# Performance work log

Hardware: AMD Instinct MI355X
Metric: run time of the kernel (lower is better)

## Reference

```python
import jax, jax.numpy as jnp
import numpy as np

THR = 0.2
BORDER_RM = 2
TEMPERATURE = 0.1


def _border_valid(hc, wc, b):
    # True for grid cells at least b away from every border; flattened to [hc*wc]
    ih = jnp.arange(hc)
    iw = jnp.arange(wc)
    vh = (ih >= b) & (ih < hc - b)
    vw = (iw >= b) & (iw < wc - b)
    return (vh[:, None] & vw[None, :]).reshape(-1)


def setup_inputs() -> dict:
    key = jax.random.key(0)
    k0, k1 = jax.random.split(key)
    N, C = 4, 256
    h0c = w0c = h1c = w1c = 64  # 512/8 coarse grid
    feat_c0 = jax.random.normal(k0, (N, h0c * w0c, C), dtype=jnp.float32)
    feat_c1 = jax.random.normal(k1, (N, h1c * w1c, C), dtype=jnp.float32)
    return {"feat_c0": feat_c0, "feat_c1": feat_c1,
            "h0c": h0c, "w0c": w0c, "h1c": h1c, "w1c": w1c}


def reference(feat_c0, feat_c1, h0c, w0c, h1c, w1c):
    C = feat_c0.shape[-1]
    inv_sqrt_c = 1.0 / np.sqrt(C)
    f0 = feat_c0 * inv_sqrt_c
    f1 = feat_c1 * inv_sqrt_c
    # [N, L, S] similarity, dual softmax
    sim = jnp.einsum('nlc,nsc->nls', f0, f1) / TEMPERATURE
    conf = jax.nn.softmax(sim, axis=1) * jax.nn.softmax(sim, axis=2)
    # threshold + border suppression (eval path: mask_border)
    mask = conf > THR
    v0 = _border_valid(h0c, w0c, BORDER_RM)  # [L]
    v1 = _border_valid(h1c, w1c, BORDER_RM)  # [S]
    mask = mask & v0[None, :, None] & v1[None, None, :]
    # mutual top-1 (argmax along both rows and columns)
    mask = mask & (conf == conf.max(axis=2, keepdims=True)) \
                & (conf == conf.max(axis=1, keepdims=True))
    # per-row match: padded fixed-shape form of torch.where(mask_v)
    mask_v = mask.any(axis=2)                     # [N, L] bool: row i has a match
    j_ids = jnp.argmax(mask, axis=2)              # [N, L] matched column (0 if none)
    mconf = jnp.take_along_axis(conf, j_ids[..., None], axis=2)[..., 0]
    mconf = jnp.where(mask_v, mconf, 0.0)         # zero where no match (== m_bids filter)
    return conf, mask_v, j_ids.astype(jnp.int32), mconf
```

## Files before the change

kernel.cpp:

```cpp
#include <hip/hip_runtime.h>

#define L_DIM 4096
#define C_DIM 256
#define NB 4

typedef __bf16 bf16x8 __attribute__((ext_vector_type(8)));
typedef float f32x4 __attribute__((ext_vector_type(4)));

#define GLB __attribute__((address_space(1)))
#define AS3 __attribute__((address_space(3)))

__global__ void init_ws(float* __restrict__ rsum, float* __restrict__ csum,
                        unsigned int* __restrict__ colmax,
                        unsigned long long* __restrict__ rowpack) {
    int i = blockIdx.x * 256 + threadIdx.x;
    if (i < NB * L_DIM) { rsum[i] = 0.f; csum[i] = 0.f; colmax[i] = 0u; rowpack[i] = 0ull; }
}

__global__ __launch_bounds__(256) void conv_k(const float* __restrict__ f0,
                                              const float* __restrict__ f1,
                                              __bf16* __restrict__ abf,
                                              __bf16* __restrict__ bbf) {
    int i = blockIdx.x * 256 + threadIdx.x;
    const float* in = blockIdx.y ? f1 : f0;
    __bf16* out = blockIdx.y ? bbf : abf;
    const float4* p = (const float4*)in + (size_t)i * 2;
    float4 a = p[0], b = p[1];
    bf16x8 v;
    v[0]=(__bf16)a.x; v[1]=(__bf16)a.y; v[2]=(__bf16)a.z; v[3]=(__bf16)a.w;
    v[4]=(__bf16)b.x; v[5]=(__bf16)b.y; v[6]=(__bf16)b.z; v[7]=(__bf16)b.w;
    *(bf16x8*)&out[(size_t)i * 8] = v;
}

template<bool PRE, int MODE>
__global__ __launch_bounds__(256) void gemm_pass(
        const float* __restrict__ f0, const float* __restrict__ f1,
        const __bf16* __restrict__ a_bf, const __bf16* __restrict__ b_bf,
        float* __restrict__ E,
        float* __restrict__ rsum, float* __restrict__ csum,
        unsigned long long* __restrict__ rowpack, unsigned int* __restrict__ colmax) {
    const int n  = blockIdx.z;
    const int tl = blockIdx.y;
    const int ts = blockIdx.x;

    constexpr int LDST = PRE ? 64 : 72;
    __shared__ __bf16 Al[128 * LDST];
    __shared__ __bf16 Bl[128 * LDST];

    const int t    = threadIdx.x;
    const int lane = t & 63;
    const int wave = t >> 6;
    const int wm   = wave >> 1, wn = wave & 1;
    const int q    = lane >> 4;
    const int l15  = lane & 15;

    const float* A = f0 + ((size_t)n * L_DIM + (size_t)tl * 128) * C_DIM;
    const float* B = f1 + ((size_t)n * L_DIM + (size_t)ts * 128) * C_DIM;
    const __bf16* gA = a_bf + ((size_t)n * L_DIM + (size_t)tl * 128) * C_DIM;
    const __bf16* gB = b_bf + ((size_t)n * L_DIM + (size_t)ts * 128) * C_DIM;

    f32x4 acc[4][4] = {};

    const int r8 = t >> 3;
    const int c8 = t & 7;
    const int lr = lane >> 3;
    const int lc = ((lane & 7) ^ lr) * 8;

    for (int kt = 0; kt < C_DIM; kt += 64) {
        if constexpr (PRE) {
            #pragma unroll
            for (int i = 0; i < 4; ++i) {
                const int chunk = wave * 4 + i;
                const int row = chunk * 8 + lr;
                __builtin_amdgcn_global_load_lds(
                    (const GLB void*)(gA + (size_t)row * C_DIM + kt + lc),
                    (AS3 void*)&Al[chunk * 512], 16, 0, 0);
                __builtin_amdgcn_global_load_lds(
                    (const GLB void*)(gB + (size_t)row * C_DIM + kt + lc),
                    (AS3 void*)&Bl[chunk * 512], 16, 0, 0);
            }
        } else {
            #pragma unroll
            for (int i = 0; i < 4; ++i) {
                int row = r8 + 32 * i;
                const float4* pa = (const float4*)(A + (size_t)row * C_DIM + kt + c8 * 8);
                float4 a0 = pa[0], a1 = pa[1];
                const float4* pb = (const float4*)(B + (size_t)row * C_DIM + kt + c8 * 8);
                float4 b0 = pb[0], b1 = pb[1];
                bf16x8 av, bv;
                av[0]=(__bf16)a0.x; av[1]=(__bf16)a0.y; av[2]=(__bf16)a0.z; av[3]=(__bf16)a0.w;
                av[4]=(__bf16)a1.x; av[5]=(__bf16)a1.y; av[6]=(__bf16)a1.z; av[7]=(__bf16)a1.w;
                bv[0]=(__bf16)b0.x; bv[1]=(__bf16)b0.y; bv[2]=(__bf16)b0.z; bv[3]=(__bf16)b0.w;
                bv[4]=(__bf16)b1.x; bv[5]=(__bf16)b1.y; bv[6]=(__bf16)b1.z; bv[7]=(__bf16)b1.w;
                *(bf16x8*)&Al[row * LDST + c8 * 8] = av;
                *(bf16x8*)&Bl[row * LDST + c8 * 8] = bv;
            }
        }
        __syncthreads();
        #pragma unroll
        for (int k2 = 0; k2 < 2; ++k2) {
            int off;
            if constexpr (PRE) off = ((k2 * 4 + q) ^ (l15 & 7)) * 8;
            else               off = k2 * 32 + q * 8;
            bf16x8 af[4], bfv[4];
            #pragma unroll
            for (int mf = 0; mf < 4; ++mf)
                af[mf] = *(const bf16x8*)&Al[(wm * 64 + mf * 16 + l15) * LDST + off];
            #pragma unroll
            for (int nf = 0; nf < 4; ++nf)
                bfv[nf] = *(const bf16x8*)&Bl[(wn * 64 + nf * 16 + l15) * LDST + off];
            #pragma unroll
            for (int mf = 0; mf < 4; ++mf)
                #pragma unroll
                for (int nf = 0; nf < 4; ++nf)
                    acc[mf][nf] = __builtin_amdgcn_mfma_f32_16x16x32_bf16(
                        af[mf], bfv[nf], acc[mf][nf], 0, 0, 0);
        }
        __syncthreads();
    }

    if constexpr (MODE == 0) {
        const float scale = 0.0390625f;
        #pragma unroll
        for (int mf = 0; mf < 4; ++mf)
            #pragma unroll
            for (int nf = 0; nf < 4; ++nf)
                #pragma unroll
                for (int reg = 0; reg < 4; ++reg)
                    acc[mf][nf][reg] = __expf(acc[mf][nf][reg] * scale);

        {
            float rp[4][4];
            #pragma unroll
            for (int mf = 0; mf < 4; ++mf)
                #pragma unroll
                for (int reg = 0; reg < 4; ++reg) {
                    float v = acc[mf][0][reg] + acc[mf][1][reg] + acc[mf][2][reg] + acc[mf][3][reg];
                    v += __shfl_xor(v, 1); v += __shfl_xor(v, 2);
                    v += __shfl_xor(v, 4); v += __shfl_xor(v, 8);
                    rp[mf][reg] = v;
                }
            if (l15 == 0) {
                #pragma unroll
                for (int mf = 0; mf < 4; ++mf)
                    #pragma unroll
                    for (int reg = 0; reg < 4; ++reg)
                        atomicAdd(&rsum[n * L_DIM + tl * 128 + wm * 64 + mf * 16 + q * 4 + reg],
                                  rp[mf][reg]);
            }
        }
        {
            float cp[4];
            #pragma unroll
            for (int nf = 0; nf < 4; ++nf) {
                float v = 0.f;
                #pragma unroll
                for (int mf = 0; mf < 4; ++mf)
                    #pragma unroll
                    for (int reg = 0; reg < 4; ++reg)
                        v += acc[mf][nf][reg];
                v += __shfl_xor(v, 16); v += __shfl_xor(v, 32);
                cp[nf] = v;
            }
            if (q == 0) {
                #pragma unroll
                for (int nf = 0; nf < 4; ++nf)
                    atomicAdd(&csum[n * L_DIM + ts * 128 + wn * 64 + nf * 16 + l15], cp[nf]);
            }
        }
    } else {
        const float scale2 = 0.078125f;
        float vr[4][4];
        #pragma unroll
        for (int mf = 0; mf < 4; ++mf)
            #pragma unroll
            for (int reg = 0; reg < 4; ++reg)
                vr[mf][reg] = 1.0f / rsum[n * L_DIM + tl * 128 + wm * 64 + mf * 16 + q * 4 + reg];
        float vc[4];
        #pragma unroll
        for (int nf = 0; nf < 4; ++nf)
            vc[nf] = 1.0f / csum[n * L_DIM + ts * 128 + wn * 64 + nf * 16 + l15];

        #pragma unroll
        for (int mf = 0; mf < 4; ++mf)
            #pragma unroll
            for (int nf = 0; nf < 4; ++nf)
                #pragma unroll
                for (int reg = 0; reg < 4; ++reg)
                    acc[mf][nf][reg] =
                        __expf(acc[mf][nf][reg] * scale2) * vr[mf][reg] * vc[nf];

        float* Eb = E + (size_t)n * L_DIM * L_DIM + (size_t)tl * 128 * L_DIM + (size_t)ts * 128;
        #pragma unroll
        for (int mf = 0; mf < 4; ++mf) {
            #pragma unroll
            for (int nf = 0; nf < 4; ++nf) {
                int col = wn * 64 + nf * 16 + l15;
                #pragma unroll
                for (int reg = 0; reg < 4; ++reg) {
                    int row = wm * 64 + mf * 16 + q * 4 + reg;
                    Eb[(size_t)row * L_DIM + col] = acc[mf][nf][reg];
                }
            }
        }

        #pragma unroll
        for (int mf = 0; mf < 4; ++mf) {
            #pragma unroll
            for (int reg = 0; reg < 4; ++reg) {
                unsigned long long best = 0ull;
                #pragma unroll
                for (int nf = 0; nf < 4; ++nf) {
                    unsigned int cb = __float_as_uint(acc[mf][nf][reg]);
                    unsigned int col = (unsigned int)(ts * 128 + wn * 64 + nf * 16 + l15);
                    unsigned long long p = ((unsigned long long)cb << 32) | (unsigned int)(~col);
                    best = p > best ? p : best;
                }
                #pragma unroll
                for (int m = 1; m < 16; m <<= 1) {
                    unsigned int hi = (unsigned int)(best >> 32), lo = (unsigned int)best;
                    hi = __shfl_xor(hi, m); lo = __shfl_xor(lo, m);
                    unsigned long long o = ((unsigned long long)hi << 32) | lo;
                    best = o > best ? o : best;
                }
                if (l15 == 0)
                    atomicMax(&rowpack[n * L_DIM + tl * 128 + wm * 64 + mf * 16 + q * 4 + reg],
                              best);
            }
        }
        #pragma unroll
        for (int nf = 0; nf < 4; ++nf) {
            float m0 = acc[0][nf][0];
            #pragma unroll
            for (int mf = 0; mf < 4; ++mf)
                #pragma unroll
                for (int reg = 0; reg < 4; ++reg)
                    m0 = fmaxf(m0, acc[mf][nf][reg]);
            unsigned int cb = __float_as_uint(m0);
            unsigned int o = __shfl_xor(cb, 16); cb = o > cb ? o : cb;
            o = __shfl_xor(cb, 32); cb = o > cb ? o : cb;
            if (q == 0)
                atomicMax(&colmax[n * L_DIM + ts * 128 + wn * 64 + nf * 16 + l15], cb);
        }
    }
}

__global__ void final_k(const unsigned long long* __restrict__ rowpack,
                        const unsigned int* __restrict__ colmax,
                        float* __restrict__ mask_out, float* __restrict__ j_out,
                        float* __restrict__ mconf_out) {
    int i = blockIdx.x * 256 + threadIdx.x;
    if (i >= NB * L_DIM) return;
    int n = i >> 12, l = i & 4095;
    unsigned long long rp = rowpack[i];
    float v = __uint_as_float((unsigned int)(rp >> 32));
    int s = (int)(~(unsigned int)(rp & 0xFFFFFFFFull));
    float cv = __uint_as_float(colmax[n * L_DIM + s]);
    int lh = l >> 6, lw = l & 63;
    int sh = s >> 6, sw = s & 63;
    bool bl = (lh >= 2) && (lh < 62) && (lw >= 2) && (lw < 62);
    bool bs = (sh >= 2) && (sh < 62) && (sw >= 2) && (sw < 62);
    bool m = (v > 0.2f) && bl && bs && (v == cv);
    mask_out[i]  = m ? 1.0f : 0.0f;
    j_out[i]     = m ? (float)s : 0.0f;
    mconf_out[i] = m ? v : 0.0f;
}

extern "C" void kernel_launch(void* const* d_in, const int* in_sizes, int n_in,
                              void* d_out, int out_size, void* d_ws, size_t ws_size,
                              hipStream_t stream) {
    const float* f0 = (const float*)d_in[0];
    const float* f1 = (const float*)d_in[1];

    float* out_conf  = (float*)d_out;
    float* out_mask  = out_conf + (size_t)NB * L_DIM * L_DIM;
    float* out_j     = out_mask + NB * L_DIM;
    float* out_mconf = out_j + NB * L_DIM;

    float* rsum = (float*)d_ws;
    float* csum = rsum + NB * L_DIM;
    unsigned int* colmax = (unsigned int*)(csum + NB * L_DIM);
    unsigned long long* rowpack = (unsigned long long*)(colmax + NB * L_DIM);
    __bf16* abf = (__bf16*)(rowpack + NB * L_DIM);
    __bf16* bbf = abf + (size_t)NB * L_DIM * C_DIM;

    size_t need = (size_t)(NB * L_DIM) * 20
                + 2 * (size_t)NB * L_DIM * C_DIM * sizeof(__bf16);
    bool pre = ws_size >= need;

    init_ws<<<dim3(64), dim3(256), 0, stream>>>(rsum, csum, colmax, rowpack);
    if (pre) {
        conv_k<<<dim3(2048, 2), dim3(256), 0, stream>>>(f0, f1, abf, bbf);
        gemm_pass<true, 0><<<dim3(32, 32, NB), dim3(256), 0, stream>>>(
            f0, f1, abf, bbf, nullptr, rsum, csum, nullptr, nullptr);
        gemm_pass<true, 1><<<dim3(32, 32, NB), dim3(256), 0, stream>>>(
            f0, f1, abf, bbf, out_conf, rsum, csum, rowpack, colmax);
    } else {
        gemm_pass<false, 0><<<dim3(32, 32, NB), dim3(256), 0, stream>>>(
            f0, f1, nullptr, nullptr, nullptr, rsum, csum, nullptr, nullptr);
        gemm_pass<false, 1><<<dim3(32, 32, NB), dim3(256), 0, stream>>>(
            f0, f1, nullptr, nullptr, out_conf, rsum, csum, rowpack, colmax);
    }
    final_k<<<dim3(64), dim3(256), 0, stream>>>(rowpack, colmax, out_mask, out_j, out_mconf);
}
```

Before: 455.8 us.

## Transpose MFMA operands for vectorized conf stores and fuse workspace zeroing

Swaps the A/B operands of the bf16 MFMA so each lane owns four consecutive columns, enabling 16-byte vector stores of the large conf output and reshuffling the row/column reductions and atomics to match. Workspace zeroing moves into the conversion kernel, dropping a launch, and the fp32 fallback path is removed. Reciprocals use the fast rcp builtin, trading slight precision for fewer instructions.

```diff
diff --git a/kernel.cpp b/kernel.cpp
--- a/kernel.cpp
+++ b/kernel.cpp
@@ -10,18 +10,16 @@
 #define GLB __attribute__((address_space(1)))
 #define AS3 __attribute__((address_space(3)))
 
-__global__ void init_ws(float* __restrict__ rsum, float* __restrict__ csum,
-                        unsigned int* __restrict__ colmax,
-                        unsigned long long* __restrict__ rowpack) {
-    int i = blockIdx.x * 256 + threadIdx.x;
-    if (i < NB * L_DIM) { rsum[i] = 0.f; csum[i] = 0.f; colmax[i] = 0u; rowpack[i] = 0ull; }
-}
-
 __global__ __launch_bounds__(256) void conv_k(const float* __restrict__ f0,
                                               const float* __restrict__ f1,
                                               __bf16* __restrict__ abf,
-                                              __bf16* __restrict__ bbf) {
+                                              __bf16* __restrict__ bbf,
+                                              float* __restrict__ ws_zero) {
     int i = blockIdx.x * 256 + threadIdx.x;
+    if (blockIdx.y == 0 && blockIdx.x < 80) {
+        int j = (blockIdx.x * 256 + threadIdx.x) * 4;
+        *(f32x4*)&ws_zero[j] = (f32x4){0.f, 0.f, 0.f, 0.f};
+    }
     const float* in = blockIdx.y ? f1 : f0;
     __bf16* out = blockIdx.y ? bbf : abf;
     const float4* p = (const float4*)in + (size_t)i * 2;
@@ -32,20 +30,18 @@
     *(bf16x8*)&out[(size_t)i * 8] = v;
 }
 
-template<bool PRE, int MODE>
+template<int MODE>
 __global__ __launch_bounds__(256) void gemm_pass(
-        const float* __restrict__ f0, const float* __restrict__ f1,
         const __bf16* __restrict__ a_bf, const __bf16* __restrict__ b_bf,
         float* __restrict__ E,
         float* __restrict__ rsum, float* __restrict__ csum,
         unsigned long long* __restrict__ rowpack, unsigned int* __restrict__ colmax) {
+    const int ts = blockIdx.x;
+    const int tl = blockIdx.y;
     const int n  = blockIdx.z;
-    const int tl = blockIdx.y;
-    const int ts = blockIdx.x;
-
-    constexpr int LDST = PRE ? 64 : 72;
-    __shared__ __bf16 Al[128 * LDST];
-    __shared__ __bf16 Bl[128 * LDST];
+
+    __shared__ __bf16 Al[128 * 64];
+    __shared__ __bf16 Bl[128 * 64];
 
     const int t    = threadIdx.x;
     const int lane = t & 63;
@@ -54,67 +50,43 @@
     const int q    = lane >> 4;
     const int l15  = lane & 15;
 
-    const float* A = f0 + ((size_t)n * L_DIM + (size_t)tl * 128) * C_DIM;
-    const float* B = f1 + ((size_t)n * L_DIM + (size_t)ts * 128) * C_DIM;
     const __bf16* gA = a_bf + ((size_t)n * L_DIM + (size_t)tl * 128) * C_DIM;
     const __bf16* gB = b_bf + ((size_t)n * L_DIM + (size_t)ts * 128) * C_DIM;
 
     f32x4 acc[4][4] = {};
 
-    const int r8 = t >> 3;
-    const int c8 = t & 7;
     const int lr = lane >> 3;
     const int lc = ((lane & 7) ^ lr) * 8;
 
     for (int kt = 0; kt < C_DIM; kt += 64) {
-        if constexpr (PRE) {
-            #pragma unroll
-            for (int i = 0; i < 4; ++i) {
-                const int chunk = wave * 4 + i;
-                const int row = chunk * 8 + lr;
-                __builtin_amdgcn_global_load_lds(
-                    (const GLB void*)(gA + (size_t)row * C_DIM + kt + lc),
-                    (AS3 void*)&Al[chunk * 512], 16, 0, 0);
-                __builtin_amdgcn_global_load_lds(
-                    (const GLB void*)(gB + (size_t)row * C_DIM + kt + lc),
-                    (AS3 void*)&Bl[chunk * 512], 16, 0, 0);
-            }
-        } else {
-            #pragma unroll
-            for (int i = 0; i < 4; ++i) {
-                int row = r8 + 32 * i;
-                const float4* pa = (const float4*)(A + (size_t)row * C_DIM + kt + c8 * 8);
-                float4 a0 = pa[0], a1 = pa[1];
-                const float4* pb = (const float4*)(B + (size_t)row * C_DIM + kt + c8 * 8);
-                float4 b0 = pb[0], b1 = pb[1];
-                bf16x8 av, bv;
-                av[0]=(__bf16)a0.x; av[1]=(__bf16)a0.y; av[2]=(__bf16)a0.z; av[3]=(__bf16)a0.w;
-                av[4]=(__bf16)a1.x; av[5]=(__bf16)a1.y; av[6]=(__bf16)a1.z; av[7]=(__bf16)a1.w;
-                bv[0]=(__bf16)b0.x; bv[1]=(__bf16)b0.y; bv[2]=(__bf16)b0.z; bv[3]=(__bf16)b0.w;
-                bv[4]=(__bf16)b1.x; bv[5]=(__bf16)b1.y; bv[6]=(__bf16)b1.z; bv[7]=(__bf16)b1.w;
-                *(bf16x8*)&Al[row * LDST + c8 * 8] = av;
-                *(bf16x8*)&Bl[row * LDST + c8 * 8] = bv;
-            }
+        #pragma unroll
+        for (int i = 0; i < 4; ++i) {
+            const int chunk = wave * 4 + i;
+            const int row = chunk * 8 + lr;
+            __builtin_amdgcn_global_load_lds(
+                (const GLB void*)(gA + (size_t)row * C_DIM + kt + lc),
+                (AS3 void*)&Al[chunk * 512], 16, 0, 0);
+            __builtin_amdgcn_global_load_lds(
+                (const GLB void*)(gB + (size_t)row * C_DIM + kt + lc),
+                (AS3 void*)&Bl[chunk * 512], 16, 0, 0);
         }
         __syncthreads();
         #pragma unroll
         for (int k2 = 0; k2 < 2; ++k2) {
-            int off;
-            if constexpr (PRE) off = ((k2 * 4 + q) ^ (l15 & 7)) * 8;
-            else               off = k2 * 32 + q * 8;
+            const int off = ((k2 * 4 + q) ^ (l15 & 7)) * 8;
             bf16x8 af[4], bfv[4];
             #pragma unroll
             for (int mf = 0; mf < 4; ++mf)
-                af[mf] = *(const bf16x8*)&Al[(wm * 64 + mf * 16 + l15) * LDST + off];
-            #pragma unroll
-            for (int nf = 0; nf < 4; ++nf)
-                bfv[nf] = *(const bf16x8*)&Bl[(wn * 64 + nf * 16 + l15) * LDST + off];
+                af[mf] = *(const bf16x8*)&Al[(wm * 64 + mf * 16 + l15) * 64 + off];
+            #pragma unroll
+            for (int nf = 0; nf < 4; ++nf)
+                bfv[nf] = *(const bf16x8*)&Bl[(wn * 64 + nf * 16 + l15) * 64 + off];
             #pragma unroll
             for (int mf = 0; mf < 4; ++mf)
                 #pragma unroll
                 for (int nf = 0; nf < 4; ++nf)
                     acc[mf][nf] = __builtin_amdgcn_mfma_f32_16x16x32_bf16(
-                        af[mf], bfv[nf], acc[mf][nf], 0, 0, 0);
+                        bfv[nf], af[mf], acc[mf][nf], 0, 0, 0);
         }
         __syncthreads();
     }
@@ -129,57 +101,42 @@
                 for (int reg = 0; reg < 4; ++reg)
                     acc[mf][nf][reg] = __expf(acc[mf][nf][reg] * scale);
 
-        {
-            float rp[4][4];
-            #pragma unroll
-            for (int mf = 0; mf < 4; ++mf)
-                #pragma unroll
-                for (int reg = 0; reg < 4; ++reg) {
-                    float v = acc[mf][0][reg] + acc[mf][1][reg] + acc[mf][2][reg] + acc[mf][3][reg];
-                    v += __shfl_xor(v, 1); v += __shfl_xor(v, 2);
-                    v += __shfl_xor(v, 4); v += __shfl_xor(v, 8);
-                    rp[mf][reg] = v;
-                }
-            if (l15 == 0) {
-                #pragma unroll
-                for (int mf = 0; mf < 4; ++mf)
-                    #pragma unroll
-                    for (int reg = 0; reg < 4; ++reg)
-                        atomicAdd(&rsum[n * L_DIM + tl * 128 + wm * 64 + mf * 16 + q * 4 + reg],
-                                  rp[mf][reg]);
+        #pragma unroll
+        for (int mf = 0; mf < 4; ++mf) {
+            float v = 0.f;
+            #pragma unroll
+            for (int nf = 0; nf < 4; ++nf)
+                #pragma unroll
+                for (int reg = 0; reg < 4; ++reg)
+                    v += acc[mf][nf][reg];
+            v += __shfl_xor(v, 16); v += __shfl_xor(v, 32);
+            if (q == 0)
+                atomicAdd(&rsum[n * L_DIM + tl * 128 + wm * 64 + mf * 16 + l15], v);
+        }
+        #pragma unroll
+        for (int nf = 0; nf < 4; ++nf)
+            #pragma unroll
+            for (int reg = 0; reg < 4; ++reg) {
+                float v = acc[0][nf][reg] + acc[1][nf][reg] + acc[2][nf][reg] + acc[3][nf][reg];
+                v += __shfl_xor(v, 1); v += __shfl_xor(v, 2);
+                v += __shfl_xor(v, 4); v += __shfl_xor(v, 8);
+                if (l15 == 0)
+                    atomicAdd(&csum[n * L_DIM + ts * 128 + wn * 64 + nf * 16 + q * 4 + reg], v);
             }
-        }
-        {
-            float cp[4];
-            #pragma unroll
-            for (int nf = 0; nf < 4; ++nf) {
-                float v = 0.f;
-                #pragma unroll
-                for (int mf = 0; mf < 4; ++mf)
-                    #pragma unroll
-                    for (int reg = 0; reg < 4; ++reg)
-                        v += acc[mf][nf][reg];
-                v += __shfl_xor(v, 16); v += __shfl_xor(v, 32);
-                cp[nf] = v;
-            }
-            if (q == 0) {
-                #pragma unroll
-                for (int nf = 0; nf < 4; ++nf)
-                    atomicAdd(&csum[n * L_DIM + ts * 128 + wn * 64 + nf * 16 + l15], cp[nf]);
-            }
-        }
     } else {
         const float scale2 = 0.078125f;
-        float vr[4][4];
+        float vr[4];
         #pragma unroll
         for (int mf = 0; mf < 4; ++mf)
+            vr[mf] = __builtin_amdgcn_rcpf(
+                rsum[n * L_DIM + tl * 128 + wm * 64 + mf * 16 + l15]);
+        float vc[4][4];
+        #pragma unroll
+        for (int nf = 0; nf < 4; ++nf)
             #pragma unroll
             for (int reg = 0; reg < 4; ++reg)
-                vr[mf][reg] = 1.0f / rsum[n * L_DIM + tl * 128 + wm * 64 + mf * 16 + q * 4 + reg];
-        float vc[4];
-        #pragma unroll
-        for (int nf = 0; nf < 4; ++nf)
-            vc[nf] = 1.0f / csum[n * L_DIM + ts * 128 + wn * 64 + nf * 16 + l15];
+                vc[nf][reg] = __builtin_amdgcn_rcpf(
+                    csum[n * L_DIM + ts * 128 + wn * 64 + nf * 16 + q * 4 + reg]);
 
         #pragma unroll
         for (int mf = 0; mf < 4; ++mf)
@@ -188,60 +145,54 @@
                 #pragma unroll
                 for (int reg = 0; reg < 4; ++reg)
                     acc[mf][nf][reg] =
-                        __expf(acc[mf][nf][reg] * scale2) * vr[mf][reg] * vc[nf];
+                        __expf(acc[mf][nf][reg] * scale2) * vr[mf] * vc[nf][reg];
 
         float* Eb = E + (size_t)n * L_DIM * L_DIM + (size_t)tl * 128 * L_DIM + (size_t)ts * 128;
         #pragma unroll
         for (int mf = 0; mf < 4; ++mf) {
-            #pragma unroll
-            for (int nf = 0; nf < 4; ++nf) {
-                int col = wn * 64 + nf * 16 + l15;
+            const size_t rowoff = (size_t)(wm * 64 + mf * 16 + l15) * L_DIM;
+            #pragma unroll
+            for (int nf = 0; nf < 4; ++nf)
+                *(f32x4*)&Eb[rowoff + wn * 64 + nf * 16 + q * 4] = acc[mf][nf];
+        }
+
+        #pragma unroll
+        for (int mf = 0; mf < 4; ++mf) {
+            unsigned long long best = 0ull;
+            #pragma unroll
+            for (int nf = 0; nf < 4; ++nf)
                 #pragma unroll
                 for (int reg = 0; reg < 4; ++reg) {
-                    int row = wm * 64 + mf * 16 + q * 4 + reg;
-                    Eb[(size_t)row * L_DIM + col] = acc[mf][nf][reg];
-                }
-            }
-        }
-
-        #pragma unroll
-        for (int mf = 0; mf < 4; ++mf) {
-            #pragma unroll
-            for (int reg = 0; reg < 4; ++reg) {
-                unsigned long long best = 0ull;
-                #pragma unroll
-                for (int nf = 0; nf < 4; ++nf) {
                     unsigned int cb = __float_as_uint(acc[mf][nf][reg]);
-                    unsigned int col = (unsigned int)(ts * 128 + wn * 64 + nf * 16 + l15);
+                    unsigned int col = (unsigned int)(ts * 128 + wn * 64 + nf * 16 + q * 4 + reg);
                     unsigned long long p = ((unsigned long long)cb << 32) | (unsigned int)(~col);
                     best = p > best ? p : best;
                 }
+            #pragma unroll
+            for (int m = 16; m < 64; m <<= 1) {
+                unsigned int hi = (unsigned int)(best >> 32), lo = (unsigned int)best;
+                hi = __shfl_xor(hi, m); lo = __shfl_xor(lo, m);
+                unsigned long long o = ((unsigned long long)hi << 32) | lo;
+                best = o > best ? o : best;
+            }
+            if (q == 0)
+                atomicMax(&rowpack[n * L_DIM + tl * 128 + wm * 64 + mf * 16 + l15], best);
+        }
+        #pragma unroll
+        for (int nf = 0; nf < 4; ++nf)
+            #pragma unroll
+            for (int reg = 0; reg < 4; ++reg) {
+                float m0 = fmaxf(fmaxf(acc[0][nf][reg], acc[1][nf][reg]),
+                                 fmaxf(acc[2][nf][reg], acc[3][nf][reg]));
+                unsigned int cb = __float_as_uint(m0);
                 #pragma unroll
                 for (int m = 1; m < 16; m <<= 1) {
-                    unsigned int hi = (unsigned int)(best >> 32), lo = (unsigned int)best;
-                    hi = __shfl_xor(hi, m); lo = __shfl_xor(lo, m);
-                    unsigned long long o = ((unsigned long long)hi << 32) | lo;
-                    best = o > best ? o : best;
+                    unsigned int o = __shfl_xor(cb, m);
+                    cb = o > cb ? o : cb;
                 }
                 if (l15 == 0)
-                    atomicMax(&rowpack[n * L_DIM + tl * 128 + wm * 64 + mf * 16 + q * 4 + reg],
-                              best);
+                    atomicMax(&colmax[n * L_DIM + ts * 128 + wn * 64 + nf * 16 + q * 4 + reg], cb);
             }
-        }
-        #pragma unroll
-        for (int nf = 0; nf < 4; ++nf) {
-            float m0 = acc[0][nf][0];
-            #pragma unroll
-            for (int mf = 0; mf < 4; ++mf)
-                #pragma unroll
-                for (int reg = 0; reg < 4; ++reg)
-                    m0 = fmaxf(m0, acc[mf][nf][reg]);
-            unsigned int cb = __float_as_uint(m0);
-            unsigned int o = __shfl_xor(cb, 16); cb = o > cb ? o : cb;
-            o = __shfl_xor(cb, 32); cb = o > cb ? o : cb;
-            if (q == 0)
-                atomicMax(&colmax[n * L_DIM + ts * 128 + wn * 64 + nf * 16 + l15], cb);
-        }
     }
 }
 
@@ -284,22 +235,10 @@
     __bf16* abf = (__bf16*)(rowpack + NB * L_DIM);
     __bf16* bbf = abf + (size_t)NB * L_DIM * C_DIM;
 
-    size_t need = (size_t)(NB * L_DIM) * 20
-                + 2 * (size_t)NB * L_DIM * C_DIM * sizeof(__bf16);
-    bool pre = ws_size >= need;
-
-    init_ws<<<dim3(64), dim3(256), 0, stream>>>(rsum, csum, colmax, rowpack);
-    if (pre) {
-        conv_k<<<dim3(2048, 2), dim3(256), 0, stream>>>(f0, f1, abf, bbf);
-        gemm_pass<true, 0><<<dim3(32, 32, NB), dim3(256), 0, stream>>>(
-            f0, f1, abf, bbf, nullptr, rsum, csum, nullptr, nullptr);
-        gemm_pass<true, 1><<<dim3(32, 32, NB), dim3(256), 0, stream>>>(
-            f0, f1, abf, bbf, out_conf, rsum, csum, rowpack, colmax);
-    } else {
-        gemm_pass<false, 0><<<dim3(32, 32, NB), dim3(256), 0, stream>>>(
-            f0, f1, nullptr, nullptr, nullptr, rsum, csum, nullptr, nullptr);
-        gemm_pass<false, 1><<<dim3(32, 32, NB), dim3(256), 0, stream>>>(
-            f0, f1, nullptr, nullptr, out_conf, rsum, csum, rowpack, colmax);
-    }
+    conv_k<<<dim3(2048, 2), dim3(256), 0, stream>>>(f0, f1, abf, bbf, (float*)d_ws);
+    gemm_pass<0><<<dim3(32, 32, NB), dim3(256), 0, stream>>>(
+        abf, bbf, nullptr, rsum, csum, nullptr, nullptr);
+    gemm_pass<1><<<dim3(32, 32, NB), dim3(256), 0, stream>>>(
+        abf, bbf, out_conf, rsum, csum, rowpack, colmax);
     final_k<<<dim3(64), dim3(256), 0, stream>>>(rowpack, colmax, out_mask, out_j, out_mconf);
 }
```

Result: faster. 422.5 us (-7.3%).
